# Performance work log

Hardware: AMD Instinct MI355X
Metric: run time of the kernel (lower is better)

Reference implementation:

```python
import jax, jax.numpy as jnp
import numpy as np

B, S, D = 2, 2048, 768
H, HD = 12, 64
PAST = 2048
MAXPOS = PAST + S  # 4096


def setup_inputs() -> dict:
    key = jax.random.key(0)
    ks = jax.random.split(key, 9)
    hidden_states = jax.random.normal(ks[0], (B, S, D), dtype=jnp.float32)
    layer_past = jax.random.normal(ks[1], (2, B, H, PAST, HD), dtype=jnp.float32)
    # GPT-2 style causal multiplicative mask over full context length
    mask = jnp.tril(jnp.ones((MAXPOS, MAXPOS), dtype=jnp.float32))[None, None, :, :]
    Wq = jax.random.normal(ks[2], (D, D), dtype=jnp.float32) * 0.02
    bq = jnp.zeros((D,), dtype=jnp.float32)
    Wk = jax.random.normal(ks[3], (D, D), dtype=jnp.float32) * 0.02
    bk = jnp.zeros((D,), dtype=jnp.float32)
    Wv = jax.random.normal(ks[4], (D, D), dtype=jnp.float32) * 0.02
    bv = jnp.zeros((D,), dtype=jnp.float32)
    return {"hidden_states": hidden_states, "layer_past": layer_past, "mask": mask,
            "Wq": Wq, "bq": bq, "Wk": Wk, "bk": bk, "Wv": Wv, "bv": bv}


def _split_heads(x):
    b, s, _ = x.shape
    return x.reshape(b, s, H, HD).transpose(0, 2, 1, 3)  # [B,H,S,HD]


def reference(hidden_states, layer_past, mask, Wq, bq, Wk, bk, Wv, bv):
    q = _split_heads(hidden_states @ Wq + bq)
    k = _split_heads(hidden_states @ Wk + bk)
    v = _split_heads(hidden_states @ Wv + bv)
    # KV-cache concat along sequence dim
    k = jnp.concatenate((layer_past[0], k), axis=-2)  # [B,H,ns,HD]
    v = jnp.concatenate((layer_past[1], v), axis=-2)
    present = jnp.stack((k, v), axis=0)
    scores = jnp.einsum('bhqd,bhkd->bhqk', q, k) / 8.0  # 8 = sqrt(64)
    nd, ns = scores.shape[-2], scores.shape[-1]
    m = mask[:, :, ns - nd:ns, :ns]
    scores = scores * m - 1e10 * (1.0 - m)
    probs = jax.nn.softmax(scores, axis=-1)  # dropout is identity at eval
    ctx = jnp.einsum('bhqk,bhkd->bhqd', probs, v)
    ctx = ctx.transpose(0, 2, 1, 3).reshape(hidden_states.shape[0], nd, H * HD)
    return ctx, present
```

## Files before the change

### kernel.cpp

```cpp
#include <hip/hip_runtime.h>


typedef unsigned short u16;
typedef __attribute__((ext_vector_type(8))) short bf16x8;
typedef __attribute__((ext_vector_type(4))) float f32x4;

#define CTXN   3145728
#define CHUNK  262144
#define PCHUNK 131072
#define SHAD_NEED ((size_t)12*1024*1024 + (size_t)2*24*64*4096*2)
#define MFMA(a,b,c) __builtin_amdgcn_mfma_f32_16x16x32_bf16(a,b,c,0,0,0)

__device__ __forceinline__ u16 f2b(float f) {
    union { float f; unsigned int i; } u; u.f = f;
    unsigned int r = u.i + 0x7fffu + ((u.i >> 16) & 1u);
    return (u16)(r >> 16);
}
__device__ __forceinline__ unsigned int pk2(float lo, float hi) {
    unsigned int lr = __float_as_uint(lo); lr += 0x7fffu + ((lr >> 16) & 1u);
    unsigned int hr = __float_as_uint(hi); hr += 0x7fffu + ((hr >> 16) & 1u);
    return __builtin_amdgcn_perm(hr, lr, 0x07060302u);
}
union U8 { unsigned int w[4]; bf16x8 v; };

__device__ __forceinline__ int vpos(int k) {
    return (k & 32) | ((k & 12) << 1) | ((k & 16) >> 2) | (k & 3);
}
__device__ __forceinline__ int vkey(int p) {
    return (p & 32) | ((p & 4) << 2) | ((p & 24) >> 1) | (p & 3);
}

__global__ __launch_bounds__(256) void prep_w(
    const float* __restrict__ Wq, const float* __restrict__ Wk,
    const float* __restrict__ Wv, u16* __restrict__ WT)
{
    __shared__ __align__(16) u16 tile[64][72];
    const float* W = blockIdx.z == 0 ? Wq : (blockIdx.z == 1 ? Wk : Wv);
    const int r0 = blockIdx.y * 64, c0 = blockIdx.x * 64;
    const int t = threadIdx.x;
#pragma unroll
    for (int i = 0; i < 2; i++) {
        int idx = t + 256 * i, r = idx >> 3, c8 = idx & 7;
        const float* src = &W[(size_t)(r0 + r) * 768 + c0 + c8 * 8];
        u16 tmp[8];
#pragma unroll
        for (int j = 0; j < 8; j++) tmp[j] = f2b(src[j]);
        *(uint4*)&tile[r][c8 * 8] = *(uint4*)tmp;
    }
    __syncthreads();
#pragma unroll
    for (int i = 0; i < 2; i++) {
        int idx = t + 256 * i, n = idx >> 3, k8 = idx & 7;
        u16 tmp[8];
#pragma unroll
        for (int j = 0; j < 8; j++) tmp[j] = tile[k8 * 8 + j][n];
        *(uint4*)&WT[((size_t)blockIdx.z * 768 + c0 + n) * 768 + r0 + k8 * 8] = *(uint4*)tmp;
    }
}

__global__ __launch_bounds__(256) void prep_h(const float* __restrict__ Hs,
                                              u16* __restrict__ Hb)
{
    size_t base = ((size_t)blockIdx.x * 256 + threadIdx.x) * 16;
    u16 tmp[16];
#pragma unroll
    for (int j = 0; j < 16; j++) tmp[j] = f2b(Hs[base + j]);
    *(uint4*)&Hb[base] = *(uint4*)tmp;
    *(uint4*)&Hb[base + 8] = *(uint4*)(tmp + 8);
}

__global__ __launch_bounds__(256) void past_prep(const float* __restrict__ past,
                                                 float* __restrict__ out,
                                                 u16* __restrict__ shad)
{
    __shared__ float Vl[64][65];
    const int bh = blockIdx.x, kb = blockIdx.y, t = threadIdx.x;
    const int key = t >> 2, qd = t & 3;
    const float* Ks = past + (size_t)bh * PCHUNK + (size_t)kb * 4096;
    const float* Vs = past + (size_t)(24 + bh) * PCHUNK + (size_t)kb * 4096;
    float* Ko = out + (size_t)CTXN + (size_t)bh * CHUNK + (size_t)kb * 4096;
    float* Vo = out + (size_t)CTXN + (size_t)(24 + bh) * CHUNK + (size_t)kb * 4096;

    float4 kv[4], vv[4];
#pragma unroll
    for (int j = 0; j < 4; j++) {
        kv[j] = *(const float4*)&Ks[key * 64 + qd * 16 + j * 4];
        vv[j] = *(const float4*)&Vs[key * 64 + qd * 16 + j * 4];
    }
#pragma unroll
    for (int j = 0; j < 4; j++) {
        *(float4*)&Ko[key * 64 + qd * 16 + j * 4] = kv[j];
        *(float4*)&Vo[key * 64 + qd * 16 + j * 4] = vv[j];
        *(float4*)&Vl[key][qd * 16 + j * 4] = vv[j];
    }
    if (shad) {
        u16* Ksh = shad + (size_t)(bh * 64 + kb) * 4096;
        const float* kf = (const float*)kv;
        u16 a[8], bb[8];
#pragma unroll
        for (int j = 0; j < 8; j++) { a[j] = f2b(kf[j]); bb[j] = f2b(kf[8 + j]); }
        *(uint4*)&Ksh[key * 64 + (((2 * qd) ^ (key & 7)) * 8)] = *(uint4*)a;
        *(uint4*)&Ksh[key * 64 + (((2 * qd + 1) ^ (key & 7)) * 8)] = *(uint4*)bb;
    }
    __syncthreads();
    if (shad) {
        u16* Vsh = shad + (size_t)(1536 + bh * 64 + kb) * 4096;
        const int d = t & 63, ph = t >> 6;
#pragma unroll
        for (int s2 = 0; s2 < 2; s2++) {
            int sp = ph * 2 + s2;
            u16 c[8];
#pragma unroll
            for (int j = 0; j < 8; j++)
                c[j] = f2b(Vl[vkey(sp * 8 + j)][d]);
            *(uint4*)&Vsh[d * 64 + ((sp ^ (d & 7)) * 8)] = *(uint4*)c;
        }
    }
}

__global__ __launch_bounds__(256) void shadow_new(const float* __restrict__ out,
                                                  u16* __restrict__ shad)
{
    __shared__ float Vl[64][65];
    const int bh = blockIdx.x, kb = blockIdx.y, t = threadIdx.x;
    const int key = t >> 2, qd = t & 3;
    const float* Ks = out + (size_t)CTXN + (size_t)bh * CHUNK + (size_t)(2048 + kb * 64) * 64;
    const float* Vs = out + (size_t)CTXN + (size_t)(24 + bh) * CHUNK + (size_t)(2048 + kb * 64) * 64;

    float4 kv[4], vv[4];
#pragma unroll
    for (int j = 0; j < 4; j++) {
        kv[j] = *(const float4*)&Ks[key * 64 + qd * 16 + j * 4];
        vv[j] = *(const float4*)&Vs[key * 64 + qd * 16 + j * 4];
    }
#pragma unroll
    for (int j = 0; j < 4; j++)
        *(float4*)&Vl[key][qd * 16 + j * 4] = vv[j];
    {
        u16* Ksh = shad + (size_t)(bh * 64 + 32 + kb) * 4096;
        const float* kf = (const float*)kv;
        u16 a[8], bb[8];
#pragma unroll
        for (int j = 0; j < 8; j++) { a[j] = f2b(kf[j]); bb[j] = f2b(kf[8 + j]); }
        *(uint4*)&Ksh[key * 64 + (((2 * qd) ^ (key & 7)) * 8)] = *(uint4*)a;
        *(uint4*)&Ksh[key * 64 + (((2 * qd + 1) ^ (key & 7)) * 8)] = *(uint4*)bb;
    }
    __syncthreads();
    {
        u16* Vsh = shad + (size_t)(1536 + bh * 64 + 32 + kb) * 4096;
        const int d = t & 63, ph = t >> 6;
#pragma unroll
        for (int s2 = 0; s2 < 2; s2++) {
            int sp = ph * 2 + s2;
            u16 c[8];
#pragma unroll
            for (int j = 0; j < 8; j++)
                c[j] = f2b(Vl[vkey(sp * 8 + j)][d]);
            *(uint4*)&Vsh[d * 64 + ((sp ^ (d & 7)) * 8)] = *(uint4*)c;
        }
    }
}

__global__ __launch_bounds__(256) void qkv_gemm(
    const u16* __restrict__ Hb, const u16* __restrict__ WT,
    const float* __restrict__ bq, const float* __restrict__ bk,
    const float* __restrict__ bv, float* out)
{
    __shared__ __align__(16) u16 Al[128][72];
    __shared__ __align__(16) u16 Bl[128][72];
    const int t = threadIdx.x, lane = t & 63, w = t >> 6;
    const int wr = w >> 1, wc = w & 1;
    const int g = lane >> 4, li = lane & 15;
    const int m0 = blockIdx.y * 128, n0 = blockIdx.x * 128;
    f32x4 acc[4][4] = {};

    for (int k0 = 0; k0 < 768; k0 += 64) {
#pragma unroll
        for (int i = 0; i < 4; i++) {
            int idx = t + 256 * i, r = idx >> 3, c8 = idx & 7;
            *(uint4*)&Al[r][c8 * 8] = *(const uint4*)&Hb[(size_t)(m0 + r) * 768 + k0 + c8 * 8];
            *(uint4*)&Bl[r][c8 * 8] = *(const uint4*)&WT[(size_t)(n0 + r) * 768 + k0 + c8 * 8];
        }
        __syncthreads();
#pragma unroll
        for (int kk = 0; kk < 64; kk += 32) {
            bf16x8 af[4], bf[4];
#pragma unroll
            for (int mi = 0; mi < 4; mi++)
                af[mi] = *(const bf16x8*)&Al[wr * 64 + mi * 16 + li][kk + g * 8];
#pragma unroll
            for (int ni = 0; ni < 4; ni++)
                bf[ni] = *(const bf16x8*)&Bl[wc * 64 + ni * 16 + li][kk + g * 8];
#pragma unroll
            for (int mi = 0; mi < 4; mi++)
#pragma unroll
                for (int ni = 0; ni < 4; ni++)
                    acc[mi][ni] = MFMA(af[mi], bf[ni], acc[mi][ni]);
        }
        __syncthreads();
    }

#pragma unroll
    for (int mi = 0; mi < 4; mi++) {
#pragma unroll
        for (int ni = 0; ni < 4; ni++) {
            int col = n0 + wc * 64 + ni * 16 + li;
            int which = col >= 1536 ? 2 : (col >= 768 ? 1 : 0);
            int c2 = col - which * 768;
            int h = c2 >> 6, hd = c2 & 63;
            float bias = which == 0 ? bq[c2] : which == 1 ? bk[c2] : bv[c2];
            int rowb = m0 + wr * 64 + mi * 16 + g * 4;
#pragma unroll
            for (int r = 0; r < 4; r++) {
                int rr = rowb + r;
                float o = acc[mi][ni][r] + bias;
                if (which == 0) {
                    out[(size_t)rr * 768 + c2] = o;
                } else {
                    int b = rr >> 11, s = rr & 2047;
                    size_t off = (size_t)CTXN +
                        ((size_t)((which - 1) * 2 + b) * 12 + h) * CHUNK +
                        (size_t)(2048 + s) * 64 + hd;
                    out[off] = o;
                }
            }
        }
    }
}

#define STAGE(buf_, it_)                                                                   \
    {                                                                                      \
        const char* gK_ = Kp + (size_t)(it_) * 8192;                                       \
        const char* gV_ = Vp + (size_t)(it_) * 8192;                                       \
        char* lds_ = ldsb + (buf_) * 16384;                                                \
        const int o_ = t * 16;                                                             \
        _Pragma("unroll")                                                                  \
        for (int i_ = 0; i_ < 2; i_++) {                                                   \
            __builtin_amdgcn_global_load_lds(                                              \
                (const __attribute__((address_space(1))) unsigned int*)(gK_ + o_ + i_ * 4096), \
                (__attribute__((address_space(3))) unsigned int*)(lds_ + o_ + i_ * 4096),  \
                16, 0, 0);                                                                 \
            __builtin_amdgcn_global_load_lds(                                              \
                (const __attribute__((address_space(1))) unsigned int*)(gV_ + o_ + i_ * 4096), \
                (__attribute__((address_space(3))) unsigned int*)(lds_ + 8192 + o_ + i_ * 4096), \
                16, 0, 0);                                                                 \
        }                                                                                  \
    }

__global__ __launch_bounds__(256, 4) void attn2(const u16* __restrict__ shad, float* out)
{
    __shared__ __align__(16) u16 KV[16384];
    const int bh = blockIdx.x;
    const int qt = 31 - blockIdx.y;
    const int b = bh / 12, h = bh - 12 * b;
    const int t = threadIdx.x, lane = t & 63, w = t >> 6;
    const int g = lane >> 4, li = lane & 15, liq = li & 7;
    char* ldsb = (char*)KV;
    const char* Kp = (const char*)(shad + (size_t)bh * 262144);
    const char* Vp = (const char*)(shad + (size_t)(1536 + bh * 64) * 4096);

    const int qw = qt * 64 + w * 16;
    const float qs = 0.125f * 1.44269504f;
    u16 qa[16];
    const float* QA = out + ((size_t)b * 2048 + qw + li) * 768 + h * 64;
#pragma unroll
    for (int j = 0; j < 8; j++) {
        qa[j]     = f2b(QA[g * 8 + j] * qs);
        qa[8 + j] = f2b(QA[32 + g * 8 + j] * qs);
    }
    bf16x8 qA0 = *(bf16x8*)qa, qA1 = *(bf16x8*)(qa + 8);

    const int koff0 = (g ^ liq) * 16, koff1 = ((4 + g) ^ liq) * 16;
    int voff[2];
#pragma unroll
    for (int ks = 0; ks < 2; ks++) voff[ks] = (((ks * 4 + g)) ^ liq) * 16;

    f32x4 o[4] = {};
    float lsum = 0.f;
    const int qloc = w * 16 + li;

    const int nkb = 33 + qt;

    STAGE(0, 0)
    __syncthreads();

    for (int it = 0; it < nkb; ++it) {
        const int buf = it & 1;
        if (it + 1 < nkb) STAGE(buf ^ 1, it + 1)

        const char* lK = ldsb + buf * 16384;
        const char* lV = lK + 8192;

        f32x4 s[4];
#pragma unroll
        for (int nt = 0; nt < 4; nt++) {
            const char* kr = lK + (nt * 16 + li) * 128;
            bf16x8 k0 = *(const bf16x8*)(kr + koff0);
            bf16x8 k1 = *(const bf16x8*)(kr + koff1);
            f32x4 a = {};
            a = MFMA(k0, qA0, a); a = MFMA(k1, qA1, a);
            s[nt] = a;
        }
        if (it == nkb - 1) {
#pragma unroll
            for (int nt = 0; nt < 4; nt++)
#pragma unroll
                for (int r = 0; r < 4; r++)
                    if (nt * 16 + 4 * g + r > qloc) s[nt][r] = -30000.f;
        }

        float ts = 0.f;
#pragma unroll
        for (int nt = 0; nt < 4; nt++)
#pragma unroll
            for (int r = 0; r < 4; r++) {
                float p = __builtin_amdgcn_exp2f(s[nt][r] - 12.0f);
                s[nt][r] = p; ts += p;
            }
        ts += __shfl_xor(ts, 16);
        ts += __shfl_xor(ts, 32);
        lsum += ts;

#pragma unroll
        for (int ks = 0; ks < 2; ks++) {
            U8 pa;
            pa.w[0] = pk2(s[2 * ks][0],     s[2 * ks][1]);
            pa.w[1] = pk2(s[2 * ks][2],     s[2 * ks][3]);
            pa.w[2] = pk2(s[2 * ks + 1][0], s[2 * ks + 1][1]);
            pa.w[3] = pk2(s[2 * ks + 1][2], s[2 * ks + 1][3]);
#pragma unroll
            for (int dt = 0; dt < 4; dt++) {
                bf16x8 vf = *(const bf16x8*)(lV + (dt * 16 + li) * 128 + voff[ks]);
                o[dt] = MFMA(pa.v, vf, o[dt]);
            }
        }
        __syncthreads();
    }

    float iv = 1.0f / lsum;
    float ia[4];
#pragma unroll
    for (int r = 0; r < 4; r++)
        ia[r] = __shfl(iv, (g << 4) + (g << 2) + r);
#pragma unroll
    for (int dt = 0; dt < 4; dt++)
#pragma unroll
        for (int r = 0; r < 4; r++) {
            size_t row = (size_t)b * 2048 + qw + 4 * g + r;
            out[row * 768 + h * 64 + dt * 16 + li] = o[dt][r] * ia[r];
        }
}

__global__ __launch_bounds__(256) void attn(float* out)
{
    __shared__ __align__(16) u16 Kl[64][72];
    __shared__ __align__(16) u16 Vt[64][72];
    __shared__ __align__(16) u16 Pl[4][16][72];
    const int bh = blockIdx.x;
    const int qt = 31 - blockIdx.y;
    const int b = bh / 12, h = bh - 12 * b;
    const int t = threadIdx.x, lane = t & 63, w = t >> 6;
    const int g = lane >> 4, li = lane & 15;
    const size_t kbase = (size_t)CTXN + (size_t)bh * CHUNK;
    const size_t vbase = kbase + (size_t)24 * CHUNK;
    const int q0 = qt * 64;

    const float* Qp = out + ((size_t)b * 2048 + q0 + w * 16 + li) * 768 + h * 64;
    u16 qa[16];
#pragma unroll
    for (int j = 0; j < 8; j++) qa[j]     = f2b(Qp[g * 8 + j]);
#pragma unroll
    for (int j = 0; j < 8; j++) qa[8 + j] = f2b(Qp[32 + g * 8 + j]);
    bf16x8 qf0 = *(bf16x8*)qa, qf1 = *(bf16x8*)(qa + 8);

    f32x4 o[4] = {};
    float mrun[4], lsum[4];
#pragma unroll
    for (int r = 0; r < 4; r++) { mrun[r] = -30000.0f; lsum[r] = 0.f; }

    const int nkb = 33 + qt;
    for (int kb = 0; kb < nkb; kb++) {
#pragma unroll
        for (int i = 0; i < 2; i++) {
            int idx = t + 256 * i, r = idx >> 3, c8 = idx & 7;
            const float* src = &out[kbase + (size_t)(kb * 64 + r) * 64 + c8 * 8];
            u16 tmp[8];
#pragma unroll
            for (int j = 0; j < 8; j++) tmp[j] = f2b(src[j]);
            *(uint4*)&Kl[r][c8 * 8] = *(uint4*)tmp;
        }
#pragma unroll
        for (int i = 0; i < 2; i++) {
            int idx = t + 256 * i, d = idx >> 3, k8 = idx & 7;
            u16 tmp[8];
#pragma unroll
            for (int j = 0; j < 8; j++)
                tmp[j] = f2b(out[vbase + (size_t)(kb * 64 + k8 * 8 + j) * 64 + d]);
            *(uint4*)&Vt[d][k8 * 8] = *(uint4*)tmp;
        }
        __syncthreads();

        f32x4 sc[4];
#pragma unroll
        for (int nt = 0; nt < 4; nt++) {
            bf16x8 kf0 = *(const bf16x8*)&Kl[nt * 16 + li][g * 8];
            bf16x8 kf1 = *(const bf16x8*)&Kl[nt * 16 + li][32 + g * 8];
            f32x4 a = {};
            a = MFMA(qf0, kf0, a);
            a = MFMA(qf1, kf1, a);
            sc[nt] = a;
        }
        const bool diag = (kb == nkb - 1);
#pragma unroll
        for (int nt = 0; nt < 4; nt++)
#pragma unroll
            for (int r = 0; r < 4; r++) {
                float s = sc[nt][r] * 0.125f;
                if (diag) {
                    int key_l = nt * 16 + li, q_l = w * 16 + g * 4 + r;
                    if (key_l > q_l) s = -30000.0f;
                }
                sc[nt][r] = s;
            }
        float alpha[4];
#pragma unroll
        for (int r = 0; r < 4; r++) {
            float tm = fmaxf(fmaxf(sc[0][r], sc[1][r]), fmaxf(sc[2][r], sc[3][r]));
#pragma unroll
            for (int off = 1; off < 16; off <<= 1) tm = fmaxf(tm, __shfl_xor(tm, off));
            float mn = fmaxf(mrun[r], tm);
            alpha[r] = __expf(mrun[r] - mn);
            mrun[r] = mn;
            float ts = 0.f;
#pragma unroll
            for (int nt = 0; nt < 4; nt++) {
                float p = __expf(sc[nt][r] - mn);
                sc[nt][r] = p;
                ts += p;
            }
#pragma unroll
            for (int off = 1; off < 16; off <<= 1) ts += __shfl_xor(ts, off);
            lsum[r] = lsum[r] * alpha[r] + ts;
        }
#pragma unroll
        for (int dt = 0; dt < 4; dt++)
#pragma unroll
            for (int r = 0; r < 4; r++) o[dt][r] *= alpha[r];

#pragma unroll
        for (int nt = 0; nt < 4; nt++)
#pragma unroll
            for (int r = 0; r < 4; r++)
                Pl[w][g * 4 + r][nt * 16 + li] = f2b(sc[nt][r]);

        bf16x8 pa0 = *(const bf16x8*)&Pl[w][li][g * 8];
        bf16x8 pa1 = *(const bf16x8*)&Pl[w][li][32 + g * 8];
#pragma unroll
        for (int dt = 0; dt < 4; dt++) {
            bf16x8 vf0 = *(const bf16x8*)&Vt[dt * 16 + li][g * 8];
            bf16x8 vf1 = *(const bf16x8*)&Vt[dt * 16 + li][32 + g * 8];
            o[dt] = MFMA(pa0, vf0, o[dt]);
            o[dt] = MFMA(pa1, vf1, o[dt]);
        }
        __syncthreads();
    }

    float inv[4];
#pragma unroll
    for (int r = 0; r < 4; r++) inv[r] = 1.0f / lsum[r];
#pragma unroll
    for (int dt = 0; dt < 4; dt++)
#pragma unroll
        for (int r = 0; r < 4; r++) {
            int q = q0 + w * 16 + g * 4 + r;
            out[((size_t)b * 2048 + q) * 768 + h * 64 + dt * 16 + li] = o[dt][r] * inv[r];
        }
}

extern "C" void kernel_launch(void* const* d_in, const int* in_sizes, int n_in,
                              void* d_out, int out_size, void* d_ws, size_t ws_size,
                              hipStream_t stream) {
    (void)in_sizes; (void)n_in; (void)out_size;
    const float* Hs   = (const float*)d_in[0];
    const float* past = (const float*)d_in[1];
    const float* Wq = (const float*)d_in[3];
    const float* bq = (const float*)d_in[4];
    const float* Wk = (const float*)d_in[5];
    const float* bk = (const float*)d_in[6];
    const float* Wv = (const float*)d_in[7];
    const float* bv = (const float*)d_in[8];
    float* out = (float*)d_out;
    u16* WT   = (u16*)d_ws;
    u16* Hb   = (u16*)((char*)d_ws + (4  << 20));
    u16* shad = (u16*)((char*)d_ws + (12 << 20));
    const bool useShadow = ws_size >= SHAD_NEED;

    prep_w<<<dim3(12, 12, 3), 256, 0, stream>>>(Wq, Wk, Wv, WT);
    prep_h<<<dim3(768), 256, 0, stream>>>(Hs, Hb);
    past_prep<<<dim3(24, 32), 256, 0, stream>>>(past, out,
                                                useShadow ? shad : (u16*)nullptr);
    qkv_gemm<<<dim3(18, 32), 256, 0, stream>>>(Hb, WT, bq, bk, bv, out);
    if (useShadow) {
        shadow_new<<<dim3(24, 32), 256, 0, stream>>>(out, shad);
        attn2<<<dim3(24, 32), 256, 0, stream>>>(shad, out);
    } else {
        attn<<<dim3(24, 32), 256, 0, stream>>>(out);
    }
}
```

Measured before the change: 265.1 us.

## Simplify bf16 packing, defer softmax row-sum reduction, split attention launch by batch

Replaces round-to-nearest-even bf16 packing in the P matrix with a cheaper add-and-truncate rounding. Moves the cross-lane row-sum shuffle out of the key loop so it runs once at the end. Changes the V-transpose thread mapping in the shadow kernels so each thread handles its own (d, segment) pair. Splits the attention launch into two half-grids by batch-head offset. Together these reduce per-iteration ALU and shuffle work, at the cost of slightly different rounding and an extra kernel launch.

Measured after the change: 281.0 us. 1.06x slower.

```diff
diff --git a/kernel.cpp b/kernel.cpp
--- a/kernel.cpp
+++ b/kernel.cpp
@@ -17,15 +17,11 @@
     return (u16)(r >> 16);
 }
 __device__ __forceinline__ unsigned int pk2(float lo, float hi) {
-    unsigned int lr = __float_as_uint(lo); lr += 0x7fffu + ((lr >> 16) & 1u);
-    unsigned int hr = __float_as_uint(hi); hr += 0x7fffu + ((hr >> 16) & 1u);
-    return __builtin_amdgcn_perm(hr, lr, 0x07060302u);
+    return __builtin_amdgcn_perm(__float_as_uint(hi) + 0x8000u,
+                                 __float_as_uint(lo) + 0x8000u, 0x07060302u);
 }
 union U8 { unsigned int w[4]; bf16x8 v; };
 
-__device__ __forceinline__ int vpos(int k) {
-    return (k & 32) | ((k & 12) << 1) | ((k & 16) >> 2) | (k & 3);
-}
 __device__ __forceinline__ int vkey(int p) {
     return (p & 32) | ((p & 4) << 2) | ((p & 24) >> 1) | (p & 3);
 }
@@ -105,10 +101,10 @@
     __syncthreads();
     if (shad) {
         u16* Vsh = shad + (size_t)(1536 + bh * 64 + kb) * 4096;
-        const int d = t & 63, ph = t >> 6;
 #pragma unroll
         for (int s2 = 0; s2 < 2; s2++) {
-            int sp = ph * 2 + s2;
+            int i2 = t + 256 * s2;
+            int d = i2 >> 3, sp = i2 & 7;
             u16 c[8];
 #pragma unroll
             for (int j = 0; j < 8; j++)
@@ -148,10 +144,10 @@
     __syncthreads();
     {
         u16* Vsh = shad + (size_t)(1536 + bh * 64 + 32 + kb) * 4096;
-        const int d = t & 63, ph = t >> 6;
 #pragma unroll
         for (int s2 = 0; s2 < 2; s2++) {
-            int sp = ph * 2 + s2;
+            int i2 = t + 256 * s2;
+            int d = i2 >> 3, sp = i2 & 7;
             u16 c[8];
 #pragma unroll
             for (int j = 0; j < 8; j++)
@@ -247,10 +243,11 @@
         }                                                                                  \
     }
 
-__global__ __launch_bounds__(256, 4) void attn2(const u16* __restrict__ shad, float* out)
+__global__ __launch_bounds__(256, 4) void attn2(const u16* __restrict__ shad, float* out,
+                                                int bh0)
 {
     __shared__ __align__(16) u16 KV[16384];
-    const int bh = blockIdx.x;
+    const int bh = bh0 + blockIdx.x;
     const int qt = 31 - blockIdx.y;
     const int b = bh / 12, h = bh - 12 * b;
     const int t = threadIdx.x, lane = t & 63, w = t >> 6;
@@ -309,17 +306,13 @@
                     if (nt * 16 + 4 * g + r > qloc) s[nt][r] = -30000.f;
         }
 
-        float ts = 0.f;
 #pragma unroll
         for (int nt = 0; nt < 4; nt++)
 #pragma unroll
             for (int r = 0; r < 4; r++) {
                 float p = __builtin_amdgcn_exp2f(s[nt][r] - 12.0f);
-                s[nt][r] = p; ts += p;
+                s[nt][r] = p; lsum += p;
             }
-        ts += __shfl_xor(ts, 16);
-        ts += __shfl_xor(ts, 32);
-        lsum += ts;
 
 #pragma unroll
         for (int ks = 0; ks < 2; ks++) {
@@ -337,6 +330,8 @@
         __syncthreads();
     }
 
+    lsum += __shfl_xor(lsum, 16);
+    lsum += __shfl_xor(lsum, 32);
     float iv = 1.0f / lsum;
     float ia[4];
 #pragma unroll
@@ -502,7 +497,8 @@
     qkv_gemm<<<dim3(18, 32), 256, 0, stream>>>(Hb, WT, bq, bk, bv, out);
     if (useShadow) {
         shadow_new<<<dim3(24, 32), 256, 0, stream>>>(out, shad);
-        attn2<<<dim3(24, 32), 256, 0, stream>>>(shad, out);
+        attn2<<<dim3(12, 32), 256, 0, stream>>>(shad, out, 0);
+        attn2<<<dim3(12, 32), 256, 0, stream>>>(shad, out, 12);
     } else {
         attn<<<dim3(24, 32), 256, 0, stream>>>(out);
     }
```
